# Kernel optimization log

Measured on AMD Instinct MI355X. Metric: run time of the kernel, lower is better.

The kernel has to match this reference:

```python
import jax, jax.numpy as jnp
import numpy as np

N_NODES = 100000
N_EDGES = 3200000
DIN, DHID, DOUT = 128, 128, 128


def setup_inputs() -> dict:
    key = jax.random.key(0)
    ks = jax.random.split(key, 8)
    x = jax.random.normal(ks[0], (N_NODES, DIN), dtype=jnp.float32)
    edge_index = jax.random.randint(ks[1], (2, N_EDGES), 0, N_NODES, dtype=jnp.int32)
    def glorot(k, fan_in, fan_out):
        s = jnp.sqrt(6.0 / (fan_in + fan_out)).astype(jnp.float32)
        return jax.random.uniform(k, (fan_in, fan_out), jnp.float32, -s, s)
    return {
        "x": x,
        "edge_index": edge_index,
        "w1": glorot(ks[2], DIN, DHID), "b1": jnp.zeros((DHID,), jnp.float32),
        "w2": glorot(ks[3], DHID, DHID), "b2": jnp.zeros((DHID,), jnp.float32),
        "w3": glorot(ks[4], DHID, DOUT), "b3": jnp.zeros((DOUT,), jnp.float32),
    }


def reference(x, edge_index, w1, b1, w2, b2, w3, b3):
    n = x.shape[0]
    # GCN normalization with self-loops (PyG gcn_norm, edge_weight = 1)
    loop = jnp.arange(n, dtype=edge_index.dtype)
    src = jnp.concatenate([edge_index[0], loop])  # [E+N]
    dst = jnp.concatenate([edge_index[1], loop])  # [E+N]
    deg = jax.ops.segment_sum(jnp.ones_like(dst, dtype=x.dtype), dst, num_segments=n)
    dinv = jnp.where(deg > 0, jax.lax.rsqrt(deg), 0.0)
    norm = dinv[src] * dinv[dst]  # [E+N]

    def gcn_conv(h, w, b):
        h = h @ w  # [N, dout]
        msg = norm[:, None] * h[src]  # gather + scale, [E+N, dout]
        agg = jax.ops.segment_sum(msg, dst, num_segments=n)  # scatter-add
        return agg + b

    h = jax.nn.relu(gcn_conv(x, w1, b1))
    h = jax.nn.relu(gcn_conv(h, w2, b2))  # dropout p=0 / eval: no-op
    h = gcn_conv(h, w3, b3)
    return jnp.sum(h, axis=0, keepdims=True) / h.shape[0]  # [1, DOUT]
```

## Files before the change

kernel.cpp:

```cpp
#include <hip/hip_runtime.h>

#define D 128
#define BSH 8
#define CAP 10240
#define CH 8192

typedef unsigned short ushort_t;
typedef unsigned int uint_t;
typedef unsigned char uchar_t;

typedef __attribute__((ext_vector_type(8))) short frag_ab;
typedef __attribute__((ext_vector_type(4))) float frag_cd;
typedef __attribute__((ext_vector_type(2))) float float2v;

union frag_u { ushort_t u[8]; frag_ab v; };


__device__ __forceinline__ float bf2f(ushort_t u) {
    union { uint_t i; float f; } v; v.i = ((uint_t)u) << 16; return v.f;
}
__device__ __forceinline__ ushort_t f2bf(float f) {
    union { float f; uint_t i; } v; v.f = f;
    uint_t u = v.i;
    u += 0x7fffu + ((u >> 16) & 1u);
    return (ushort_t)(u >> 16);
}

__launch_bounds__(512)
__global__ void k_bin(const int* __restrict__ src, const int* __restrict__ dst,
                      int* __restrict__ curA, int* __restrict__ curB,
                      uint_t* __restrict__ binA, uint_t* __restrict__ binB,
                      int E, int nb) {
    __shared__ int hA[512], hB[512], bA[512], bB[512];
    int tx = threadIdx.x;
    for (int i = tx; i < nb; i += 512) { hA[i] = 0; hB[i] = 0; }
    __syncthreads();

    int e0 = blockIdx.x * CH;
    int e1 = min(e0 + CH, E);

    for (int e = e0 + tx; e < e1; e += 512) {
        atomicAdd(&hA[dst[e] >> BSH], 1);
        atomicAdd(&hB[src[e] >> BSH], 1);
    }
    __syncthreads();
    for (int i = tx; i < nb; i += 512) {
        bA[i] = hA[i] ? atomicAdd(&curA[i], hA[i]) : 0;
        bB[i] = hB[i] ? atomicAdd(&curB[i], hB[i]) : 0;
        hA[i] = 0; hB[i] = 0;
    }
    __syncthreads();
    for (int e = e0 + tx; e < e1; e += 512) {
        int s = src[e], d = dst[e];
        int ka = d >> BSH, kb = s >> BSH;
        int pa = bA[ka] + atomicAdd(&hA[ka], 1);
        int pb = bB[kb] + atomicAdd(&hB[kb], 1);
        if (pa < CAP) binA[(size_t)ka * CAP + pa] = ((uint_t)s << 8) | (uint_t)(d & 255);
        if (pb < CAP) binB[(size_t)kb * CAP + pb] = ((uint_t)d << 8) | (uint_t)(s & 255);
    }
}

__launch_bounds__(1024)
__global__ void k_csr(const uint_t* __restrict__ binA, const int* __restrict__ curA,
                      float* __restrict__ dinv, int* __restrict__ row_beg,
                      int* __restrict__ row_end, int* __restrict__ csr_src, int N) {
    __shared__ int hist[256];
    __shared__ int scan[256];
    int b = blockIdx.x;
    int tx = threadIdx.x;
    int cnt = min(curA[b], CAP);
    const uint_t* eb = binA + (size_t)b * CAP;

    if (tx < 256) hist[tx] = 0;
    __syncthreads();
    for (int e = tx; e < cnt; e += 1024)
        atomicAdd(&hist[eb[e] & 255u], 1);
    __syncthreads();
    int v = 0;
    if (tx < 256) { v = hist[tx]; scan[tx] = v; }
    __syncthreads();
    for (int dd = 1; dd < 256; dd <<= 1) {
        int t = 0;
        if (tx < 256 && tx >= dd) t = scan[tx - dd];
        __syncthreads();
        if (tx < 256) scan[tx] += t;
        __syncthreads();
    }
    if (tx < 256) {
        int my_excl = scan[tx] - v;
        int node = b * 256 + tx;
        if (node < N) {
            dinv[node] = rsqrtf((float)(v + 1));
            row_beg[node] = b * CAP + my_excl;
            row_end[node] = b * CAP + my_excl + v;
        }
        hist[tx] = my_excl;
    }
    __syncthreads();
    for (int e = tx; e < cnt; e += 1024) {
        uint_t pk = eb[e];
        int pos = b * CAP + atomicAdd(&hist[pk & 255u], 1);
        csr_src[pos] = (int)(pk >> 8);
    }
}

__global__ void k_wpack(const float* __restrict__ W1, const float* __restrict__ W2,
                        ushort_t* __restrict__ h1, ushort_t* __restrict__ l1,
                        ushort_t* __restrict__ h2, ushort_t* __restrict__ l2,
                        const float* __restrict__ b1, const float* __restrict__ b2,
                        float* __restrict__ bp1, float* __restrict__ bp2) {
    if (blockIdx.x == 128) {
        int p = threadIdx.x;
        if (p < 128) {
            int c = (p & 7) * 16 + (p >> 3);
            bp1[p] = b1[c];
            bp2[p] = b2[c];
        }
        return;
    }
    int gid = blockIdx.x * 256 + threadIdx.x;
    int which = gid >> 14;
    int idx = gid & 16383;
    int k = idx >> 7, n = idx & 127;
    float w = which ? W2[(((k & 7) * 16) + (k >> 3)) * 128 + n] : W1[idx];
    ushort_t h = f2bf(w);
    ushort_t l = f2bf(w - bf2f(h));
    int c = k >> 5, quad = (k >> 3) & 3, jj = k & 7;
    int j = n >> 4, l16 = n & 15;
    int lane = quad * 16 + l16;
    int dest = ((c * 8 + j) * 64 + lane) * 8 + jj;
    if (which) { h2[dest] = h; l2[dest] = l; }
    else       { h1[dest] = h; l1[dest] = l; }
}

template <int IN_F32>
__launch_bounds__(256)
__global__ void gemm_mfma(const void* __restrict__ Av, const ushort_t* __restrict__ Whi,
                          const ushort_t* __restrict__ Wlo, const float* __restrict__ dinv,
                          uchar_t* __restrict__ C8, int nrows) {
    int wave = threadIdx.x >> 6;
    int lane = threadIdx.x & 63;
    int quad = lane >> 4, l16 = lane & 15;
    int base = blockIdx.x * 128 + wave * 32;

    frag_cd acc[2][8];
#pragma unroll
    for (int rt = 0; rt < 2; rt++)
#pragma unroll
        for (int j = 0; j < 8; j++) acc[rt][j] = (frag_cd)0.f;

    const ushort_t* Ab = (const ushort_t*)Av;
    const float* Af = (const float*)Av;

#pragma unroll
    for (int c = 0; c < 4; c++) {
        frag_ab afrag[2];
        int koff = c * 32 + quad * 8;
#pragma unroll
        for (int rt = 0; rt < 2; rt++) {
            int row = min(base + rt * 16 + l16, nrows - 1);
            if (IN_F32) {
                const float* ap = Af + (size_t)row * D + koff;
                float4 a0 = *(const float4*)ap;
                float4 a1 = *(const float4*)(ap + 4);
                frag_u fu;
                fu.u[0] = f2bf(a0.x); fu.u[1] = f2bf(a0.y);
                fu.u[2] = f2bf(a0.z); fu.u[3] = f2bf(a0.w);
                fu.u[4] = f2bf(a1.x); fu.u[5] = f2bf(a1.y);
                fu.u[6] = f2bf(a1.z); fu.u[7] = f2bf(a1.w);
                afrag[rt] = fu.v;
            } else {
                afrag[rt] = *(const frag_ab*)(Ab + (size_t)row * D + koff);
            }
        }
#pragma unroll
        for (int j = 0; j < 8; j++) {
            frag_ab bh = *(const frag_ab*)(Whi + (((c * 8 + j) * 64 + lane) * 8));
            frag_ab bl = *(const frag_ab*)(Wlo + (((c * 8 + j) * 64 + lane) * 8));
#pragma unroll
            for (int rt = 0; rt < 2; rt++) {
                acc[rt][j] = __builtin_amdgcn_mfma_f32_16x16x32_bf16(afrag[rt], bh,
                                                                     acc[rt][j], 0, 0, 0);
                acc[rt][j] = __builtin_amdgcn_mfma_f32_16x16x32_bf16(afrag[rt], bl,
                                                                     acc[rt][j], 0, 0, 0);
            }
        }
    }

#pragma unroll
    for (int rt = 0; rt < 2; rt++) {
        int rbase = base + rt * 16 + quad * 4;
#pragma unroll
        for (int reg = 0; reg < 4; reg++) {
            int row = rbase + reg;
            if (row < nrows) {
                float dv = dinv[row];
                uint_t d0 = (uint_t)__builtin_amdgcn_cvt_pk_fp8_f32(
                    acc[rt][0][reg] * dv, acc[rt][1][reg] * dv, 0, false);
                d0 = (uint_t)__builtin_amdgcn_cvt_pk_fp8_f32(
                    acc[rt][2][reg] * dv, acc[rt][3][reg] * dv, (int)d0, true);
                uint_t d1 = (uint_t)__builtin_amdgcn_cvt_pk_fp8_f32(
                    acc[rt][4][reg] * dv, acc[rt][5][reg] * dv, 0, false);
                d1 = (uint_t)__builtin_amdgcn_cvt_pk_fp8_f32(
                    acc[rt][6][reg] * dv, acc[rt][7][reg] * dv, (int)d1, true);
                uint2 o; o.x = d0; o.y = d1;
                *(uint2*)(C8 + (size_t)row * D + l16 * 8) = o;
            }
        }
    }
}

__launch_bounds__(256)
__global__ void agg8(const uint_t* __restrict__ t8, const int* __restrict__ csr_src,
                     const int* __restrict__ row_beg, const int* __restrict__ row_end,
                     const float* __restrict__ dinv, const float* __restrict__ bias,
                     uint_t* __restrict__ out, int n, int do_relu) {
    int node = blockIdx.x * 4 + (threadIdx.x >> 6);
    if (node >= n) return;
    int lane = threadIdx.x & 63;
    int eh = lane >> 5;
    uint_t cl = (uint_t)(lane & 31);

    int beg = row_beg[node];
    int deg = row_end[node] - beg;
    float dn = dinv[node];

    float2v accA = {0.f, 0.f}, accB = {0.f, 0.f};

    if (eh == 0) {
        uint_t w = t8[(uint_t)node * 32u + cl];
        accA = __builtin_amdgcn_cvt_pk_f32_fp8(w, false);
        accB = __builtin_amdgcn_cvt_pk_f32_fp8(w, true);
    }

    int h0 = (deg + 1) >> 1;
    int e = beg + (eh ? h0 : 0);
    int eend = beg + (eh ? deg : h0);
    for (; e + 7 < eend; e += 8) {
        uint4 sa, sb;
        __builtin_memcpy(&sa, csr_src + e, 16);
        __builtin_memcpy(&sb, csr_src + e + 4, 16);
        uint_t w0 = t8[sa.x * 32u + cl];
        uint_t w1 = t8[sa.y * 32u + cl];
        uint_t w2 = t8[sa.z * 32u + cl];
        uint_t w3 = t8[sa.w * 32u + cl];
        uint_t w4 = t8[sb.x * 32u + cl];
        uint_t w5 = t8[sb.y * 32u + cl];
        uint_t w6 = t8[sb.z * 32u + cl];
        uint_t w7 = t8[sb.w * 32u + cl];
        accA += __builtin_amdgcn_cvt_pk_f32_fp8(w0, false);
        accB += __builtin_amdgcn_cvt_pk_f32_fp8(w0, true);
        accA += __builtin_amdgcn_cvt_pk_f32_fp8(w1, false);
        accB += __builtin_amdgcn_cvt_pk_f32_fp8(w1, true);
        accA += __builtin_amdgcn_cvt_pk_f32_fp8(w2, false);
        accB += __builtin_amdgcn_cvt_pk_f32_fp8(w2, true);
        accA += __builtin_amdgcn_cvt_pk_f32_fp8(w3, false);
        accB += __builtin_amdgcn_cvt_pk_f32_fp8(w3, true);
        accA += __builtin_amdgcn_cvt_pk_f32_fp8(w4, false);
        accB += __builtin_amdgcn_cvt_pk_f32_fp8(w4, true);
        accA += __builtin_amdgcn_cvt_pk_f32_fp8(w5, false);
        accB += __builtin_amdgcn_cvt_pk_f32_fp8(w5, true);
        accA += __builtin_amdgcn_cvt_pk_f32_fp8(w6, false);
        accB += __builtin_amdgcn_cvt_pk_f32_fp8(w6, true);
        accA += __builtin_amdgcn_cvt_pk_f32_fp8(w7, false);
        accB += __builtin_amdgcn_cvt_pk_f32_fp8(w7, true);
    }
    for (; e + 3 < eend; e += 4) {
        uint4 ss;
        __builtin_memcpy(&ss, csr_src + e, 16);
        uint_t w0 = t8[ss.x * 32u + cl];
        uint_t w1 = t8[ss.y * 32u + cl];
        uint_t w2 = t8[ss.z * 32u + cl];
        uint_t w3 = t8[ss.w * 32u + cl];
        accA += __builtin_amdgcn_cvt_pk_f32_fp8(w0, false);
        accB += __builtin_amdgcn_cvt_pk_f32_fp8(w0, true);
        accA += __builtin_amdgcn_cvt_pk_f32_fp8(w1, false);
        accB += __builtin_amdgcn_cvt_pk_f32_fp8(w1, true);
        accA += __builtin_amdgcn_cvt_pk_f32_fp8(w2, false);
        accB += __builtin_amdgcn_cvt_pk_f32_fp8(w2, true);
        accA += __builtin_amdgcn_cvt_pk_f32_fp8(w3, false);
        accB += __builtin_amdgcn_cvt_pk_f32_fp8(w3, true);
    }
    for (; e < eend; ++e) {
        uint_t s = (uint_t)csr_src[e];
        uint_t w = t8[s * 32u + cl];
        accA += __builtin_amdgcn_cvt_pk_f32_fp8(w, false);
        accB += __builtin_amdgcn_cvt_pk_f32_fp8(w, true);
    }

    float a0 = accA.x, a1 = accA.y, a2 = accB.x, a3 = accB.y;
    a0 += __shfl(a0, lane ^ 32, 64);
    a1 += __shfl(a1, lane ^ 32, 64);
    a2 += __shfl(a2, lane ^ 32, 64);
    a3 += __shfl(a3, lane ^ 32, 64);

    if (eh == 0) {
        float4 bb = ((const float4*)bias)[cl];
        float o0 = dn * a0 + bb.x;
        float o1 = dn * a1 + bb.y;
        float o2 = dn * a2 + bb.z;
        float o3 = dn * a3 + bb.w;
        if (do_relu) {
            o0 = fmaxf(o0, 0.f); o1 = fmaxf(o1, 0.f);
            o2 = fmaxf(o2, 0.f); o3 = fmaxf(o3, 0.f);
        }
        uint2 ow;
        ow.x = (uint_t)f2bf(o0) | ((uint_t)f2bf(o1) << 16);
        ow.y = (uint_t)f2bf(o2) | ((uint_t)f2bf(o3) << 16);
        ((uint2*)out)[(size_t)node * 32 + cl] = ow;
    }
}

__launch_bounds__(512)
__global__ void wreduce(const ushort_t* __restrict__ h, const uint_t* __restrict__ binB,
                        const int* __restrict__ curB, const float* __restrict__ dinv,
                        float* __restrict__ v, int n) {
    __shared__ float owacc[256];
    __shared__ float s[512];
    int b = blockIdx.x;
    int tx = threadIdx.x;
    if (tx < 256) owacc[tx] = 0.f;
    __syncthreads();
    int cnt = min(curB[b], CAP);
    const uint_t* eb = binB + (size_t)b * CAP;
    for (int e = tx; e < cnt; e += 512) {
        uint_t pk = eb[e];
        atomicAdd(&owacc[pk & 255u], dinv[pk >> 8]);
    }
    __syncthreads();

    int c = tx & 127;
    int rg = tx >> 7;
    int base = b * 256;
    int lim = min(base + 256, n);
    float acc = 0.f;
    for (int r = base + rg; r < lim; r += 4) {
        float dv = dinv[r];
        float cv = dv * (dv + owacc[r - base]);
        acc += cv * bf2f(h[(size_t)r * D + c]);
    }
    s[tx] = acc;
    __syncthreads();
    if (tx < 128)
        atomicAdd(&v[c], (s[tx] + s[tx + 128]) + (s[tx + 256] + s[tx + 384]));
}

__global__ void finalize(const float* __restrict__ v, const float* __restrict__ w3,
                         const float* __restrict__ b3, float* __restrict__ out, float invn) {
    __shared__ float sv[D];
    int j = threadIdx.x;
    sv[j] = v[j];
    __syncthreads();
    float acc = 0.f;
    for (int k = 0; k < D; k++) {
        int p = (k & 15) * 8 + (k >> 4);
        acc += sv[p] * w3[(size_t)k * D + j];
    }
    out[j] = acc * invn + b3[j];
}

extern "C" void kernel_launch(void* const* d_in, const int* in_sizes, int n_in,
                              void* d_out, int out_size, void* d_ws, size_t ws_size,
                              hipStream_t stream) {
    const float* x   = (const float*)d_in[0];
    const int*   ei  = (const int*)d_in[1];
    const float* w1  = (const float*)d_in[2];
    const float* b1  = (const float*)d_in[3];
    const float* w2  = (const float*)d_in[4];
    const float* b2  = (const float*)d_in[5];
    const float* w3  = (const float*)d_in[6];
    const float* b3  = (const float*)d_in[7];
    float* out = (float*)d_out;

    const int N = in_sizes[0] / D;
    const int E = in_sizes[1] / 2;
    const int* src = ei;
    const int* dst = ei + E;
    const int nb = (N + 255) >> 8;

    char* p = (char*)d_ws;
    auto alloc = [&](size_t bytes) -> char* {
        char* r = p;
        p += (bytes + 255) & ~(size_t)255;
        return r;
    };
    char*     zbeg     = p;
    int*      curA     = (int*)alloc(512 * 4);
    int*      curB     = (int*)alloc(512 * 4);
    float*    v        = (float*)alloc((size_t)D * 4);
    char*     zend     = p;
    float*    dinv     = (float*)alloc((size_t)N * 4);
    int*      row_beg  = (int*)alloc((size_t)N * 4);
    int*      row_end  = (int*)alloc((size_t)N * 4);
    ushort_t* wp1h     = (ushort_t*)alloc(16384 * 2);
    ushort_t* wp1l     = (ushort_t*)alloc(16384 * 2);
    ushort_t* wp2h     = (ushort_t*)alloc(16384 * 2);
    ushort_t* wp2l     = (ushort_t*)alloc(16384 * 2);
    float*    bp1      = (float*)alloc(D * 4);
    float*    bp2      = (float*)alloc(D * 4);
    uint_t*   binA     = (uint_t*)alloc((size_t)nb * CAP * 4);
    uint_t*   binB     = (uint_t*)alloc((size_t)nb * CAP * 4);
    int*      csr_src  = (int*)alloc((size_t)nb * CAP * 4);
    ushort_t* bufH     = (ushort_t*)alloc((size_t)N * D * 2);
    uint_t*   buf8     = (uint_t*)alloc((size_t)N * 32 * 4);
    (void)ws_size;

    const int gG = (N + 127) / 128;

    hipMemsetAsync(zbeg, 0, (size_t)(zend - zbeg), stream);

    k_wpack<<<129, 256, 0, stream>>>(w1, w2, wp1h, wp1l, wp2h, wp2l, b1, b2, bp1, bp2);

    k_bin<<<(E + CH - 1) / CH, 512, 0, stream>>>(src, dst, curA, curB, binA, binB, E, nb);
    k_csr<<<nb, 1024, 0, stream>>>(binA, curA, dinv, row_beg, row_end, csr_src, N);

    gemm_mfma<1><<<gG, 256, 0, stream>>>(x, wp1h, wp1l, dinv, (uchar_t*)buf8, N);
    agg8<<<(N + 3) / 4, 256, 0, stream>>>(buf8, csr_src, row_beg, row_end, dinv, bp1,
                                          (uint_t*)bufH, N, 1);
    gemm_mfma<0><<<gG, 256, 0, stream>>>(bufH, wp2h, wp2l, dinv, (uchar_t*)buf8, N);
    agg8<<<(N + 3) / 4, 256, 0, stream>>>(buf8, csr_src, row_beg, row_end, dinv, bp2,
                                          (uint_t*)bufH, N, 1);
    wreduce<<<nb, 512, 0, stream>>>(bufH, binB, curB, dinv, v, N);
    finalize<<<1, D, 0, stream>>>(v, w3, b3, out, 1.0f / (float)N);
}
```

Measured before the change: 428.1 us.

## Stage binned edges in shared memory for coalesced bucket writes

The edge-binning kernel now does a block-local prefix scan over bucket counts, scatters each edge into a shared-memory staging array sorted by bucket, and then writes out contiguously per bucket. The goal is to replace the scattered single-word global writes with mostly contiguous runs, improving write coalescing. In exchange it adds several barrier-heavy scans, processes the A and B bins in two sequential passes that each reread src/dst, and uses about 48KB of shared memory per block, which can lower occupancy. It also assumes nb is at most 512, since hA/hB are now indexed directly by thread id.

New measurement: 399.9 us. 6.6% less time.

```diff
diff --git a/kernel.cpp b/kernel.cpp
--- a/kernel.cpp
+++ b/kernel.cpp
@@ -31,32 +31,80 @@
                       int* __restrict__ curA, int* __restrict__ curB,
                       uint_t* __restrict__ binA, uint_t* __restrict__ binB,
                       int E, int nb) {
-    __shared__ int hA[512], hB[512], bA[512], bB[512];
+    __shared__ int hA[512], hB[512], sc[512], gb[512];
+    __shared__ ushort_t sbkt[CH];
+    __shared__ uint_t sent[CH];
     int tx = threadIdx.x;
-    for (int i = tx; i < nb; i += 512) { hA[i] = 0; hB[i] = 0; }
+    hA[tx] = 0; hB[tx] = 0;
     __syncthreads();
 
     int e0 = blockIdx.x * CH;
     int e1 = min(e0 + CH, E);
+    int total = e1 - e0;
 
     for (int e = e0 + tx; e < e1; e += 512) {
         atomicAdd(&hA[dst[e] >> BSH], 1);
         atomicAdd(&hB[src[e] >> BSH], 1);
     }
     __syncthreads();
-    for (int i = tx; i < nb; i += 512) {
-        bA[i] = hA[i] ? atomicAdd(&curA[i], hA[i]) : 0;
-        bB[i] = hB[i] ? atomicAdd(&curB[i], hB[i]) : 0;
-        hA[i] = 0; hB[i] = 0;
-    }
-    __syncthreads();
-    for (int e = e0 + tx; e < e1; e += 512) {
-        int s = src[e], d = dst[e];
-        int ka = d >> BSH, kb = s >> BSH;
-        int pa = bA[ka] + atomicAdd(&hA[ka], 1);
-        int pb = bB[kb] + atomicAdd(&hB[kb], 1);
-        if (pa < CAP) binA[(size_t)ka * CAP + pa] = ((uint_t)s << 8) | (uint_t)(d & 255);
-        if (pb < CAP) binB[(size_t)kb * CAP + pb] = ((uint_t)d << 8) | (uint_t)(s & 255);
+
+    {
+        int v = hA[tx];
+        sc[tx] = v;
+        __syncthreads();
+        for (int d = 1; d < 512; d <<= 1) {
+            int t = (tx >= d) ? sc[tx - d] : 0;
+            __syncthreads();
+            sc[tx] += t;
+            __syncthreads();
+        }
+        sc[tx] -= v;
+        gb[tx] = v ? atomicAdd(&curA[tx], v) : 0;
+        hA[tx] = 0;
+        __syncthreads();
+        for (int e = e0 + tx; e < e1; e += 512) {
+            int s = src[e], d = dst[e];
+            int k = d >> BSH;
+            int pos = sc[k] + atomicAdd(&hA[k], 1);
+            sent[pos] = ((uint_t)s << 8) | (uint_t)(d & 255);
+            sbkt[pos] = (ushort_t)k;
+        }
+        __syncthreads();
+        for (int p = tx; p < total; p += 512) {
+            int k = sbkt[p];
+            int gp = gb[k] + (p - sc[k]);
+            if (gp < CAP) binA[(size_t)k * CAP + gp] = sent[p];
+        }
+        __syncthreads();
+    }
+
+    {
+        int v = hB[tx];
+        sc[tx] = v;
+        __syncthreads();
+        for (int d = 1; d < 512; d <<= 1) {
+            int t = (tx >= d) ? sc[tx - d] : 0;
+            __syncthreads();
+            sc[tx] += t;
+            __syncthreads();
+        }
+        sc[tx] -= v;
+        gb[tx] = v ? atomicAdd(&curB[tx], v) : 0;
+        hB[tx] = 0;
+        __syncthreads();
+        for (int e = e0 + tx; e < e1; e += 512) {
+            int s = src[e], d = dst[e];
+            int k = s >> BSH;
+            int pos = sc[k] + atomicAdd(&hB[k], 1);
+            sent[pos] = ((uint_t)d << 8) | (uint_t)(s & 255);
+            sbkt[pos] = (ushort_t)k;
+        }
+        __syncthreads();
+        for (int p = tx; p < total; p += 512) {
+            int k = sbkt[p];
+            int gp = gb[k] + (p - sc[k]);
+            if (gp < CAP) binB[(size_t)k * CAP + gp] = sent[p];
+        }
     }
 }
 
```
